# Optimization experiments

Hardware: AMD Instinct MI355X
Metric: run time of the kernel (lower is better)

Reference implementation:

```python
import jax, jax.numpy as jnp
import numpy as np
from jax import lax

B, N, H, D = 4, 384, 8, 5          # graphs, nodes/graph, heads, max multi-hop dist
NE, E_TOT, DH, L = 2048, 8192, 256, 10  # edges/graph, total real edges, d_hidden, curve samples
N_SPATIAL, N_EDGE_DIST = 64, 128


def _bn(x, g, b):
    # eval-mode BatchNorm1d (running_mean=0, running_var=1): affine only
    return x * g + b


def _conv1d(x, w):
    # x: [E, C, L], w: [O, I, 3], SAME padding, stride 1
    return lax.conv_general_dilated(x, w, (1,), 'SAME',
                                    dimension_numbers=('NCH', 'OIH', 'NCH'))


def setup_inputs() -> dict:
    key = jax.random.key(0)
    ks = iter(jax.random.split(key, 64))
    nrm = lambda shape, s=0.02: jax.random.normal(next(ks), shape, jnp.float32) * s
    std = 0.02 / np.sqrt(12.0)  # init_params with n_layer=12 for Linear weights
    inp = {}
    inp['attn_bias'] = jax.random.normal(next(ks), (B, N + 1, N + 1), jnp.float32)
    inp['spatial_pos'] = jax.random.randint(next(ks), (B, N, N), 0, N_SPATIAL)
    inp['d2_dist'] = jax.random.normal(next(ks), (B, N, N, 32), jnp.float32)
    inp['a3_dist'] = jax.random.normal(next(ks), (B, N, N, 32), jnp.float32)
    inp['edge_data'] = jax.random.normal(next(ks), (E_TOT, L, 7), jnp.float32)
    inp['edge_path'] = jax.random.randint(next(ks), (B, N, N, D), 0, NE + 1)
    inp['edge_padding_mask'] = jnp.zeros((B, NE), bool)  # all real edges
    inp['src'] = jax.random.randint(next(ks), (E_TOT,), 0, B * N)
    inp['dst'] = jax.random.randint(next(ks), (E_TOT,), 0, B * N)
    inp['node_data'] = jax.random.normal(next(ks), (B * N, DH), jnp.float32)
    # --- parameters ---
    inp['spatial_emb'] = nrm((N_SPATIAL, H)).at[0].set(0.0)  # padding_idx=0
    inp['t_virtual'] = nrm((1, H))
    inp['w_d2'] = nrm((H, 32), std); inp['b_d2'] = jnp.zeros((H,), jnp.float32)
    inp['w_a3'] = nrm((H, 32), std); inp['b_a3'] = jnp.zeros((H,), jnp.float32)
    inp['cw1'] = nrm((64, 7, 3), std);  inp['cg1'] = jnp.ones((64,));  inp['cb1'] = jnp.zeros((64,))
    inp['cw2'] = nrm((128, 64, 3), std); inp['cg2'] = jnp.ones((128,)); inp['cb2'] = jnp.zeros((128,))
    inp['cw3'] = nrm((256, 128, 3), std); inp['cg3'] = jnp.ones((256,)); inp['cb3'] = jnp.zeros((256,))
    inp['cw_out'] = nrm((H, 256), std)
    # _EdgeConv (UV-Net style): proj Linear(d_hidden->H), MLP(H->64->H), BN, GIN eps
    inp['wp'] = nrm((H, DH), std); inp['bp'] = jnp.zeros((H,))
    inp['w1'] = nrm((64, H), std); inp['b1'] = jnp.zeros((64,))
    inp['g1'] = jnp.ones((64,)); inp['bb1'] = jnp.zeros((64,))
    inp['w2'] = nrm((H, 64), std); inp['b2'] = jnp.zeros((H,))
    inp['g_out'] = jnp.ones((H,)); inp['bb_out'] = jnp.zeros((H,))
    inp['eps'] = jnp.zeros((), jnp.float32)
    inp['edge_dis_w'] = nrm((N_EDGE_DIST * H * H, 1))
    return inp


def reference(attn_bias, spatial_pos, d2_dist, a3_dist, edge_data, edge_path,
              edge_padding_mask, src, dst, node_data, spatial_emb, t_virtual,
              w_d2, b_d2, w_a3, b_a3, cw1, cg1, cb1, cw2, cg2, cb2, cw3, cg3, cb3,
              cw_out, wp, bp, w1, b1, g1, bb1, w2, b2, g_out, bb_out, eps, edge_dis_w):
    gab = jnp.repeat(attn_bias[:, None], H, axis=1)            # [B,H,N+1,N+1]
    spb = spatial_emb[spatial_pos]                              # [B,N,N,H]
    d2b = d2_dist @ w_d2.T + b_d2                               # [B,N,N,H]
    a3b = a3_dist @ w_a3.T + b_a3                               # [B,N,N,H]
    # CurveEncoder on per-edge curve samples
    x = jnp.transpose(edge_data, (0, 2, 1))                     # [E,7,L]
    x = jax.nn.leaky_relu(_bn(_conv1d(x, cw1), cg1[:, None], cb1[:, None]))
    x = jax.nn.leaky_relu(_bn(_conv1d(x, cw2), cg2[:, None], cb2[:, None]))
    x = jax.nn.leaky_relu(_bn(_conv1d(x, cw3), cg3[:, None], cb3[:, None]))
    ef = jnp.mean(x, axis=-1) @ cw_out.T                        # [E,H]
    # _EdgeConv: combine endpoint node features with edge features
    proj = node_data @ wp.T + bp                                # [B*N,H]
    h = (1.0 + eps) * ef + proj[src] + proj[dst]
    h = jax.nn.relu(_bn(h @ w1.T + b1, g1, bb1)) @ w2.T + b2
    edge_out = jax.nn.relu(_bn(h, g_out, bb_out))               # [E,H]
    # scatter real-edge features into padded table (row NE stays zero = padding)
    valid = (~edge_padding_mask).reshape(-1)                    # [B*NE]
    gidx = jnp.maximum(jnp.cumsum(valid) - 1, 0)
    vals = jnp.where(valid[:, None], edge_out[gidx], 0.0).reshape(B, NE, H)
    edge_feature = jnp.zeros((B, NE + 1, H), edge_out.dtype).at[:, :NE].set(vals)
    # gather along multi-hop paths, per-distance head mixing (bmm), normalize
    ep = edge_path.reshape(B, N * N * D)
    edge_input = jax.vmap(lambda f, p: f[p])(edge_feature, ep)  # [B,N*N*D,H]
    edge_input = edge_input.reshape(B, N, N, D, H)
    wdis = edge_dis_w.reshape(-1, H, H)[:D]                     # [D,H,H]
    edge_input = jnp.einsum('bijdh,dhk->bijdk', edge_input, wdis)
    sp = jnp.where(spatial_pos == 0, 1, spatial_pos)
    sp = jnp.where(sp > 1, sp - 1, sp)
    sp = jnp.clip(sp, 0, D)
    edge_bias = edge_input.sum(-2) / sp[..., None].astype(edge_input.dtype)
    inner = spb + d2b + a3b + edge_bias                         # [B,N,N,H]
    gab = gab.at[:, :, 1:, 1:].add(jnp.transpose(inner, (0, 3, 1, 2)))
    t = t_virtual.reshape(1, H, 1)
    gab = gab.at[:, :, 1:, 0].add(t)
    gab = gab.at[:, :, 0, :].add(t)
    return gab + attn_bias[:, None]
```

## Files before the change

### kernel.cpp

```cpp
#include <hip/hip_runtime.h>

#define NB    4
#define NNODE 384
#define NH    8
#define ND    5
#define NEDGE 2048
#define NEP1  2049
#define ETOT  8192
#define DHID  256
#define NP1   385
#define SQ1   (NP1*NP1)
#define NPOS  98304
#define NPOS2 (NPOS + 2)
#define NCELL (NB*NNODE*NNODE)

typedef __attribute__((ext_vector_type(8)))  short short8;
typedef __attribute__((ext_vector_type(16))) float float16;

__device__ __forceinline__ unsigned short f2bf(float f) {
    union { float f; unsigned int u; } v; v.f = f;
    unsigned int u = v.u;
    return (unsigned short)((u + 0x7FFFu + ((u >> 16) & 1u)) >> 16);
}
__device__ __forceinline__ float bf2f(unsigned short s) {
    union { unsigned int u; float f; } v; v.u = ((unsigned int)s) << 16; return v.f;
}
__device__ __forceinline__ unsigned pkbf(float a, float b) {
    return (unsigned)f2bf(a) | ((unsigned)f2bf(b) << 16);
}
__device__ __forceinline__ short8 mk8(unsigned a, unsigned b, unsigned c, unsigned d) {
    union { unsigned u[4]; short8 s; } x; x.u[0]=a; x.u[1]=b; x.u[2]=c; x.u[3]=d; return x.s;
}
__device__ __forceinline__ float leaky(float v) { return v > 0.f ? v : 0.01f * v; }
__device__ __forceinline__ float16 zero16() {
    float16 z;
#pragma unroll
    for (int i = 0; i < 16; ++i) z[i] = 0.f;
    return z;
}
__device__ __forceinline__ void gl_lds16(const void* g, void* l) {
    __builtin_amdgcn_global_load_lds(
        (const __attribute__((address_space(1))) unsigned int*)g,
        (__attribute__((address_space(3))) unsigned int*)l,
        16, 0, 0);
}

__global__ __launch_bounds__(256) void prep_kernel(
    const float* __restrict__ cw1, const float* __restrict__ cw2, const float* __restrict__ cw3,
    const float* __restrict__ cw_out,
    const float* __restrict__ node_data, const float* __restrict__ wp, const float* __restrict__ bp,
    unsigned short* __restrict__ W1f, unsigned short* __restrict__ W2f, unsigned short* __restrict__ W3f,
    unsigned short* __restrict__ Wof,
    float* __restrict__ proj, float* __restrict__ edge_feature)
{
    int gid = blockIdx.x * 256 + threadIdx.x;
    if (gid < 98304) {
        int j = gid & 7, lane = (gid >> 3) & 63, blk = gid >> 9;
        int ks = blk & 7, tp = (blk >> 3) % 3, mt = blk / 24;
        int oc = mt * 32 + (lane & 31);
        int ic = ks * 16 + (lane >> 5) * 8 + j;
        W3f[gid] = f2bf(cw3[(oc * 128 + ic) * 3 + tp]);
    } else if (gid < 122880) {
        int f = gid - 98304;
        int j = f & 7, lane = (f >> 3) & 63, blk = f >> 9;
        int ks = blk & 3, tp = (blk >> 2) % 3, mt = blk / 12;
        int oc = mt * 32 + (lane & 31);
        int ic = ks * 16 + (lane >> 5) * 8 + j;
        W2f[f] = f2bf(cw2[(oc * 64 + ic) * 3 + tp]);
    } else if (gid < 124928) {
        int f = gid - 122880;
        int j = f & 7, lane = (f >> 3) & 63, blk = f >> 9;
        int ks = blk & 1, mt = blk >> 1;
        int oc = mt * 32 + (lane & 31);
        int k = ks * 16 + (lane >> 5) * 8 + j;
        int tp = k >> 3, c = k & 7;
        float v = (tp < 3 && c < 7) ? cw1[oc * 21 + c * 3 + tp] : 0.f;
        W1f[f] = f2bf(v);
    } else if (gid < 137216) {
        int f = gid - 124928;
        int v = f >> 3, h = f & 7;
        const float4* nd4 = (const float4*)(node_data + (size_t)v * DHID);
        const float4* ww4 = (const float4*)(wp + (size_t)h * DHID);
        float s0 = 0.f, s1 = 0.f, s2 = 0.f, s3 = 0.f;
#pragma unroll 4
        for (int c = 0; c < 64; c += 4) {
            float4 x0 = nd4[c+0], y0 = ww4[c+0];
            float4 x1 = nd4[c+1], y1 = ww4[c+1];
            float4 x2 = nd4[c+2], y2 = ww4[c+2];
            float4 x3 = nd4[c+3], y3 = ww4[c+3];
            s0 += x0.x*y0.x + x0.y*y0.y + x0.z*y0.z + x0.w*y0.w;
            s1 += x1.x*y1.x + x1.y*y1.y + x1.z*y1.z + x1.w*y1.w;
            s2 += x2.x*y2.x + x2.y*y2.y + x2.z*y2.z + x2.w*y2.w;
            s3 += x3.x*y3.x + x3.y*y3.y + x3.z*y3.z + x3.w*y3.w;
        }
        proj[f] = bp[h] + (s0 + s1) + (s2 + s3);
    } else if (gid < 137248) {
        int f = gid - 137216;
        int b = f >> 3, h = f & 7;
        edge_feature[((size_t)b * NEP1 + NEDGE) * NH + h] = 0.f;
    } else if (gid < 145440) {
        int f = gid - 137248;
        int j = f & 7, lane = (f >> 3) & 63, g = f >> 9;
        int m = lane & 31;
        int k = g * 16 + (lane >> 5) * 8 + j;
        Wof[f] = (m < 8) ? f2bf(cw_out[m * 256 + k]) : (unsigned short)0;
    }
}

#define X0_GROWS 8
__global__ __launch_bounds__(256) void pack_kernel(
    const float* __restrict__ edge_data,
    unsigned short* __restrict__ X0buf, unsigned short* __restrict__ X1buf,
    unsigned short* __restrict__ X2buf)
{
    int gid = blockIdx.x * 256 + threadIdx.x;
    const int NX0 = (NPOS + 2 * X0_GROWS) * 8;
    if (gid < NX0) {
        int row = gid >> 3, ch = gid & 7;
        int pos = row - X0_GROWS;
        unsigned short v = 0;
        if (pos >= 0 && pos < NPOS && ch < 7) {
            int pm = pos % 12;
            if (pm >= 1 && pm <= 10)
                v = f2bf(edge_data[(size_t)(pos / 12) * 70 + (pm - 1) * 7 + ch]);
        }
        X0buf[gid] = v;
    } else if (gid < NX0 + 128) {
        int f = gid - NX0;
        int p = f >> 5, rest = f & 31;
        int row = (rest >> 4) ? (NPOS + 1) : 0, col = rest & 15;
        X1buf[((size_t)p * NPOS2 + row) * 16 + col] = 0;
    } else if (gid < NX0 + 128 + 256) {
        int f = gid - NX0 - 128;
        int p = f >> 5, rest = f & 31;
        int row = (rest >> 4) ? (NPOS + 1) : 0, col = rest & 15;
        X2buf[((size_t)p * NPOS2 + row) * 16 + col] = 0;
    }
}

__global__ __launch_bounds__(256, 4) void conv1_kernel(
    const unsigned short* __restrict__ X0, const unsigned short* __restrict__ W1f,
    const float* __restrict__ cg1, const float* __restrict__ cb1,
    unsigned short* __restrict__ X1)
{
    const int t = threadIdx.x, wv = t >> 6, lane = t & 63;
    const int q = lane >> 5, n = lane & 31;
    const int pos = blockIdx.x * 128 + wv * 32 + n;

    float16 acc0 = zero16(), acc1 = zero16();
#pragma unroll
    for (int ks = 0; ks < 2; ++ks) {
        short8 b  = *(const short8*)(X0 + (pos - 1 + 2 * ks + q) * 8);
        short8 a0 = *(const short8*)(W1f + ((0 * 2 + ks) * 64 + lane) * 8);
        short8 a1 = *(const short8*)(W1f + ((1 * 2 + ks) * 64 + lane) * 8);
        acc0 = __builtin_amdgcn_mfma_f32_32x32x16_bf16(a0, b, acc0, 0, 0, 0);
        acc1 = __builtin_amdgcn_mfma_f32_32x32x16_bf16(a1, b, acc1, 0, 0, 0);
    }
    int pm = pos % 12;
    bool valid = (pm != 0) && (pm != 11);
#pragma unroll
    for (int mt = 0; mt < 2; ++mt) {
        const float16& acc = mt ? acc1 : acc0;
#pragma unroll
        for (int r2 = 0; r2 < 4; ++r2) {
            int oc0 = mt * 32 + 8 * r2 + 4 * q;
            float4 g4 = *(const float4*)(cg1 + oc0);
            float4 b4 = *(const float4*)(cb1 + oc0);
            unsigned short uu[4];
            uu[0] = valid ? f2bf(leaky(acc[r2*4+0] * g4.x + b4.x)) : (unsigned short)0;
            uu[1] = valid ? f2bf(leaky(acc[r2*4+1] * g4.y + b4.y)) : (unsigned short)0;
            uu[2] = valid ? f2bf(leaky(acc[r2*4+2] * g4.z + b4.z)) : (unsigned short)0;
            uu[3] = valid ? f2bf(leaky(acc[r2*4+3] * g4.w + b4.w)) : (unsigned short)0;
            uint2 pk; pk.x = uu[0] | ((unsigned)uu[1] << 16); pk.y = uu[2] | ((unsigned)uu[3] << 16);
            *(uint2*)(void*)(X1 + ((size_t)(oc0 >> 4) * NPOS2 + pos + 1) * 16 + (oc0 & 15)) = pk;
        }
    }
}

__global__ __launch_bounds__(256, 4) void conv2_kernel(
    const unsigned short* __restrict__ X1, const unsigned short* __restrict__ W2f,
    const float* __restrict__ cg2, const float* __restrict__ cb2,
    unsigned short* __restrict__ X2)
{
    __shared__ __align__(16) unsigned short sB[4][1568];
    const int t = threadIdx.x, wv = t >> 6, lane = t & 63;
    const int q = lane >> 5, n = lane & 31;
    const int base = blockIdx.x * 96;
    const int cbase = (wv < 3) ? wv * 64 : 132;

#pragma unroll
    for (int ks = 0; ks < 4; ++ks)
        gl_lds16(X1 + ((size_t)ks * NPOS2 + base) * 16 + (cbase + lane) * 8,
                 &sB[ks][cbase * 8]);

    float16 acc[3];
#pragma unroll
    for (int nt = 0; nt < 3; ++nt) acc[nt] = zero16();

    __syncthreads();

#pragma unroll
    for (int ks = 0; ks < 4; ++ks)
#pragma unroll
        for (int tp = 0; tp < 3; ++tp) {
            short8 a = *(const short8*)(W2f + (((wv * 3 + tp) * 4 + ks) * 64 + lane) * 8);
#pragma unroll
            for (int nt = 0; nt < 3; ++nt) {
                short8 b = *(const short8*)(&sB[ks][(nt * 32 + n + tp) * 16 + q * 8]);
                acc[nt] = __builtin_amdgcn_mfma_f32_32x32x16_bf16(a, b, acc[nt], 0, 0, 0);
            }
        }

#pragma unroll
    for (int nt = 0; nt < 3; ++nt) {
        int pos = base + nt * 32 + n;
        int pm = pos % 12;
        bool valid = (pm != 0) && (pm != 11);
#pragma unroll
        for (int r2 = 0; r2 < 4; ++r2) {
            int oc0 = wv * 32 + 8 * r2 + 4 * q;
            float4 g4 = *(const float4*)(cg2 + oc0);
            float4 b4 = *(const float4*)(cb2 + oc0);
            unsigned short uu[4];
            uu[0] = valid ? f2bf(leaky(acc[nt][r2*4+0] * g4.x + b4.x)) : (unsigned short)0;
            uu[1] = valid ? f2bf(leaky(acc[nt][r2*4+1] * g4.y + b4.y)) : (unsigned short)0;
            uu[2] = valid ? f2bf(leaky(acc[nt][r2*4+2] * g4.z + b4.z)) : (unsigned short)0;
            uu[3] = valid ? f2bf(leaky(acc[nt][r2*4+3] * g4.w + b4.w)) : (unsigned short)0;
            uint2 pk; pk.x = uu[0] | ((unsigned)uu[1] << 16); pk.y = uu[2] | ((unsigned)uu[3] << 16);
            *(uint2*)(void*)(X2 + ((size_t)(oc0 >> 4) * NPOS2 + pos + 1) * 16 + (oc0 & 15)) = pk;
        }
    }
}

__global__ __launch_bounds__(256, 3) void conv3_kernel(
    const unsigned short* __restrict__ X2, const unsigned short* __restrict__ W3f,
    const unsigned short* __restrict__ Wof,
    const float* __restrict__ cg3, const float* __restrict__ cb3,
    const int* __restrict__ src, const int* __restrict__ dst,
    const float* __restrict__ w1, const float* __restrict__ b1,
    const float* __restrict__ g1, const float* __restrict__ bb1,
    const float* __restrict__ w2, const float* __restrict__ b2,
    const float* __restrict__ g_out, const float* __restrict__ bb_out,
    const float* __restrict__ eps, const float* __restrict__ proj,
    float* __restrict__ edge_feature)
{
    __shared__ __align__(16) unsigned char smem3[25088];
    unsigned short* sB = (unsigned short*)smem3;
    float* fs = (float*)smem3;
    const int t = threadIdx.x, wv = t >> 6, lane = t & 63;
    const int q = lane >> 5, n = lane & 31;
    const int base = blockIdx.x * 96;
    const int cbase = (wv < 3) ? wv * 64 : 132;

#pragma unroll
    for (int ks = 0; ks < 8; ++ks)
        gl_lds16(X2 + ((size_t)ks * NPOS2 + base) * 16 + (cbase + lane) * 8,
                 &sB[ks * 1568 + cbase * 8]);

    float16 acc[2][3];
#pragma unroll
    for (int i = 0; i < 2; ++i)
#pragma unroll
        for (int nt = 0; nt < 3; ++nt) acc[i][nt] = zero16();

    __syncthreads();

#pragma unroll
    for (int ks = 0; ks < 8; ++ks)
#pragma unroll
        for (int tp = 0; tp < 3; ++tp) {
            short8 a0 = *(const short8*)(W3f + ((((wv*2+0) * 3 + tp) * 8 + ks) * 64 + lane) * 8);
            short8 a1 = *(const short8*)(W3f + ((((wv*2+1) * 3 + tp) * 8 + ks) * 64 + lane) * 8);
#pragma unroll
            for (int nt = 0; nt < 3; ++nt) {
                short8 b = *(const short8*)(&sB[ks * 1568 + (nt * 32 + n + tp) * 16 + q * 8]);
                acc[0][nt] = __builtin_amdgcn_mfma_f32_32x32x16_bf16(a0, b, acc[0][nt], 0, 0, 0);
                acc[1][nt] = __builtin_amdgcn_mfma_f32_32x32x16_bf16(a1, b, acc[1][nt], 0, 0, 0);
            }
        }

    __syncthreads();

    short8 wof[4];
#pragma unroll
    for (int g = 0; g < 4; ++g)
        wof[g] = *(const short8*)(Wof + ((wv * 4 + g) * 64 + lane) * 8);

#pragma unroll
    for (int nt = 0; nt < 3; ++nt) {
        int pm = (nt * 32 + n) % 12;
        bool valid = (pm != 0) && (pm != 11);
        float16 p = zero16();
#pragma unroll
        for (int i = 0; i < 2; ++i) {
            int mt = wv * 2 + i;
            float av[16];
#pragma unroll
            for (int r2 = 0; r2 < 4; ++r2) {
                int oc0 = mt * 32 + 8 * r2 + 4 * q;
                float4 g4 = *(const float4*)(cg3 + oc0);
                float4 b4 = *(const float4*)(cb3 + oc0);
                av[r2*4+0] = valid ? leaky(acc[i][nt][r2*4+0] * g4.x + b4.x) : 0.f;
                av[r2*4+1] = valid ? leaky(acc[i][nt][r2*4+1] * g4.y + b4.y) : 0.f;
                av[r2*4+2] = valid ? leaky(acc[i][nt][r2*4+2] * g4.z + b4.z) : 0.f;
                av[r2*4+3] = valid ? leaky(acc[i][nt][r2*4+3] * g4.w + b4.w) : 0.f;
            }
            unsigned pk[8], op[8];
#pragma unroll
            for (int z = 0; z < 8; ++z) pk[z] = pkbf(av[2*z], av[2*z+1]);
#pragma unroll
            for (int z = 0; z < 8; ++z) op[z] = __shfl_xor((int)pk[z], 32);
            short8 f0 = q == 0 ? mk8(pk[0], pk[1], op[0], op[1])
                               : mk8(op[2], op[3], pk[2], pk[3]);
            short8 f1 = q == 0 ? mk8(pk[4], pk[5], op[4], op[5])
                               : mk8(op[6], op[7], pk[6], pk[7]);
            p = __builtin_amdgcn_mfma_f32_32x32x16_bf16(wof[i*2+0], f0, p, 0, 0, 0);
            p = __builtin_amdgcn_mfma_f32_32x32x16_bf16(wof[i*2+1], f1, p, 0, 0, 0);
        }
        float4 st = make_float4(p[0], p[1], p[2], p[3]);
        *(float4*)&fs[((wv * 96) + nt * 32 + n) * 8 + 4 * q] = st;
    }
    __syncthreads();

    if (t < 64) {
        int e = t >> 3, h = t & 7;
        float s = 0.f;
#pragma unroll
        for (int w = 0; w < 4; ++w)
#pragma unroll 4
            for (int l = 0; l < 12; ++l) s += fs[(w * 96 + e * 12 + l) * 8 + h];
        float efv = 0.1f * s;
        int ge = blockIdx.x * 8 + e;
        fs[3072 + e * 8 + h] = (1.f + eps[0]) * efv
                             + proj[src[ge] * NH + h] + proj[dst[ge] * NH + h];
    }
    __syncthreads();

#pragma unroll
    for (int bb = 0; bb < 512; bb += 256) {
        int idx = bb + t;
        int e = idx >> 6, o = idx & 63;
        float a = b1[o];
#pragma unroll
        for (int h = 0; h < 8; ++h) a += fs[3072 + e * 8 + h] * w1[o * 8 + h];
        float v = a * g1[o] + bb1[o];
        fs[3136 + e * 64 + o] = v > 0.f ? v : 0.f;
    }
    __syncthreads();

    if (t < 64) {
        int e = t >> 3, h = t & 7;
        float a = b2[h];
#pragma unroll 8
        for (int o = 0; o < 64; ++o) a += fs[3136 + e * 64 + o] * w2[h * 64 + o];
        float v = a * g_out[h] + bb_out[h];
        v = v > 0.f ? v : 0.f;
        int ge = blockIdx.x * 8 + e;
        int b = ge >> 11, el2 = ge & (NEDGE - 1);
        edge_feature[((size_t)b * NEP1 + el2) * NH + h] = v;
    }
}

__global__ __launch_bounds__(256) void eins_kernel(
    const float* __restrict__ d2_dist, const float* __restrict__ a3_dist,
    const float* __restrict__ w_d2, const float* __restrict__ w_a3,
    unsigned short* __restrict__ acc8)
{
    __shared__ __align__(16) float s_wd2[256];
    __shared__ __align__(16) float s_wa3[256];
    int t = threadIdx.x;
    s_wd2[t] = w_d2[t]; s_wa3[t] = w_a3[t];
    __syncthreads();

    const int part = t & 7;
    const bool pb0 = part & 1, pb1 = (part >> 1) & 1, pb2 = (part >> 2) & 1;
    size_t cell = (size_t)blockIdx.x * 32 + (t >> 3);

    float4 vd = ((const float4*)(d2_dist + cell * 32))[part];
    float4 va = ((const float4*)(a3_dist + cell * 32))[part];

    float acc[8];
#pragma unroll
    for (int h = 0; h < 8; ++h) {
        float4 w4 = ((const float4*)s_wd2)[h * 8 + part];
        float4 v4 = ((const float4*)s_wa3)[h * 8 + part];
        acc[h] = vd.x*w4.x + vd.y*w4.y + vd.z*w4.z + vd.w*w4.w
               + va.x*v4.x + va.y*v4.y + va.z*v4.z + va.w*v4.w;
    }
    float y0 = (pb0 ? acc[1] : acc[0]) + __shfl_xor(pb0 ? acc[0] : acc[1], 1, 64);
    float y1 = (pb0 ? acc[3] : acc[2]) + __shfl_xor(pb0 ? acc[2] : acc[3], 1, 64);
    float y2 = (pb0 ? acc[5] : acc[4]) + __shfl_xor(pb0 ? acc[4] : acc[5], 1, 64);
    float y3 = (pb0 ? acc[7] : acc[6]) + __shfl_xor(pb0 ? acc[6] : acc[7], 1, 64);
    float z0 = (pb1 ? y1 : y0) + __shfl_xor(pb1 ? y0 : y1, 2, 64);
    float z1 = (pb1 ? y3 : y2) + __shfl_xor(pb1 ? y2 : y3, 2, 64);
    float rr = (pb2 ? z1 : z0) + __shfl_xor(pb2 ? z0 : z1, 4, 64);

    acc8[cell * 8 + part] = f2bf(rr);
}

__global__ __launch_bounds__(256) void tbl_kernel(
    const float* __restrict__ edge_feature, const float* __restrict__ edge_dis_w,
    float* __restrict__ T)
{
    int idx = blockIdx.x * 256 + threadIdx.x;
    if (idx >= NEP1 * 8) return;
    int pi = idx >> 3, k = idx & 7;
    int d = blockIdx.y, b = blockIdx.z;
    const float* ef = edge_feature + ((size_t)b * NEP1 + pi) * NH;
    const float* w  = edge_dis_w + d * 64 + k;
    float s = 0.f;
#pragma unroll
    for (int h = 0; h < 8; ++h) s += ef[h] * w[h * 8];
    T[(((size_t)b * ND + d) * NEP1 + pi) * 8 + k] = s;
}

__global__ __launch_bounds__(256) void bias_kernel(
    const float* __restrict__ attn_bias, const int* __restrict__ spatial_pos,
    const int* __restrict__ edge_path,
    const float* __restrict__ spatial_emb, const float* __restrict__ t_virtual,
    const float* __restrict__ b_d2, const float* __restrict__ b_a3,
    const float* __restrict__ Tbl, const unsigned short* __restrict__ acc8,
    float* __restrict__ out)
{
    __shared__ float s_emb[512];
    __shared__ float s_t[8], s_bd2[8], s_ba3[8];

    int t = threadIdx.x;
    for (int i = t; i < 512; i += 256) s_emb[i] = spatial_emb[i];
    if (t < 8) { s_t[t] = t_virtual[t]; s_bd2[t] = b_d2[t]; s_ba3[t] = b_a3[t]; }
    __syncthreads();

    int gc = blockIdx.x * 32 + (t >> 3);
    int part = t & 7;
    if (gc >= NB * SQ1) return;
    int b   = gc / SQ1;
    int rem = gc % SQ1;
    int i = rem / NP1, j = rem % NP1;

    float base = 2.f * attn_bias[gc];
    bool border = (i == 0) || (j == 0);
    int r = border ? 0 : i - 1, c = border ? 0 : j - 1;
    size_t nidx = ((size_t)b * NNODE + r) * NNODE + c;
    int sp = spatial_pos[nidx];

    float accv = bf2f(acc8[nidx * 8 + part]);

    float edp = 0.f;
    const int* ep = edge_path + nidx * ND;
    const float* Tb = Tbl + (size_t)b * (ND * NEP1 * 8);
#pragma unroll
    for (int d = 0; d < ND; ++d) {
        int pi = ep[d];
        edp += Tb[((size_t)d * NEP1 + pi) * 8 + part];
    }
    int spd = (sp == 0) ? 1 : sp;
    spd = (spd > 1) ? spd - 1 : spd;
    spd = (spd > ND) ? ND : spd;
    float inv = 1.f / (float)spd;

    float val = border ? (base + s_t[part])
                       : (base + accv + edp * inv
                          + s_emb[sp * 8 + part] + s_bd2[part] + s_ba3[part]);
    out[((size_t)b * NH + part) * SQ1 + (size_t)i * NP1 + j] = val;
}

extern "C" void kernel_launch(void* const* d_in, const int* in_sizes, int n_in,
                              void* d_out, int out_size, void* d_ws, size_t ws_size,
                              hipStream_t stream)
{
    const float* attn_bias   = (const float*)d_in[0];
    const int*   spatial_pos = (const int*)  d_in[1];
    const float* d2_dist     = (const float*)d_in[2];
    const float* a3_dist     = (const float*)d_in[3];
    const float* edge_data   = (const float*)d_in[4];
    const int*   edge_path   = (const int*)  d_in[5];
    const int*   src         = (const int*)  d_in[7];
    const int*   dst         = (const int*)  d_in[8];
    const float* node_data   = (const float*)d_in[9];
    const float* spatial_emb = (const float*)d_in[10];
    const float* t_virtual   = (const float*)d_in[11];
    const float* w_d2        = (const float*)d_in[12];
    const float* b_d2        = (const float*)d_in[13];
    const float* w_a3        = (const float*)d_in[14];
    const float* b_a3        = (const float*)d_in[15];
    const float* cw1         = (const float*)d_in[16];
    const float* cg1         = (const float*)d_in[17];
    const float* cb1         = (const float*)d_in[18];
    const float* cw2         = (const float*)d_in[19];
    const float* cg2         = (const float*)d_in[20];
    const float* cb2         = (const float*)d_in[21];
    const float* cw3         = (const float*)d_in[22];
    const float* cg3         = (const float*)d_in[23];
    const float* cb3         = (const float*)d_in[24];
    const float* cw_out      = (const float*)d_in[25];
    const float* wp          = (const float*)d_in[26];
    const float* bp          = (const float*)d_in[27];
    const float* w1          = (const float*)d_in[28];
    const float* b1          = (const float*)d_in[29];
    const float* g1          = (const float*)d_in[30];
    const float* bb1         = (const float*)d_in[31];
    const float* w2          = (const float*)d_in[32];
    const float* b2          = (const float*)d_in[33];
    const float* g_out       = (const float*)d_in[34];
    const float* bb_out      = (const float*)d_in[35];
    const float* eps         = (const float*)d_in[36];
    const float* edge_dis_w  = (const float*)d_in[37];

    float*          proj  = (float*)d_ws;
    float*          ef    = proj + NB * NNODE * NH;
    unsigned short* W1f   = (unsigned short*)(ef + NB * NEP1 * NH);
    unsigned short* W2f   = W1f + 2048;
    unsigned short* W3f   = W2f + 24576;
    unsigned short* Wof   = W3f + 98304;
    unsigned short* X0buf = Wof + 8192;
    unsigned short* X1buf = X0buf + (size_t)(NPOS + 2 * X0_GROWS) * 8;
    unsigned short* X2buf = X1buf + (size_t)4 * NPOS2 * 16;
    unsigned short* X0 = X0buf + X0_GROWS * 8;
    float*          Tbl   = (float*)X0buf;
    unsigned short* acc8  = X1buf;

    prep_kernel<<<569, 256, 0, stream>>>(cw1, cw2, cw3, cw_out, node_data, wp, bp,
                                         W1f, W2f, W3f, Wof, proj, ef);
    pack_kernel<<<3074, 256, 0, stream>>>(edge_data, X0buf, X1buf, X2buf);

    conv1_kernel<<<NPOS / 128, 256, 0, stream>>>(X0, W1f, cg1, cb1, X1buf);
    conv2_kernel<<<NPOS / 96, 256, 0, stream>>>(X1buf, W2f, cg2, cb2, X2buf);

    eins_kernel<<<NCELL / 32, 256, 0, stream>>>(d2_dist, a3_dist, w_d2, w_a3, acc8);

    conv3_kernel<<<NPOS / 96, 256, 0, stream>>>(X2buf, W3f, Wof, cg3, cb3,
                                                src, dst, w1, b1, g1, bb1,
                                                w2, b2, g_out, bb_out, eps,
                                                proj, ef);

    dim3 tgrid((NEP1 * 8 + 255) / 256, ND, NB);
    tbl_kernel<<<tgrid, 256, 0, stream>>>(ef, edge_dis_w, Tbl);

    int nbias = (NB * SQ1 * 8 + 255) / 256;
    bias_kernel<<<nbias, 256, 0, stream>>>(
        attn_bias, spatial_pos, edge_path,
        spatial_emb, t_virtual, b_d2, b_a3,
        Tbl, acc8, (float*)d_out);
}
```

Measured before the change: 370.1 us.

## Make einsum kernel persistent with register weights and prefetch; one cell per bias thread

The d2/a3 einsum kernel now keeps its weights in registers instead of shared memory. It runs a grid-stride loop over 8 cells per thread and prefetches the next cell's inputs. The bias kernel now assigns one output cell per thread instead of one head per thread. That thread reads all 8 heads with vector loads of acc8 and the Tbl rows, which cuts repeated index loads (spatial_pos, edge_path, attn_bias) by a factor of 8. The cost is that the eight output stores per thread are strided by SQ1 across heads, and more registers are used per thread.

```diff
diff --git a/kernel.cpp b/kernel.cpp
--- a/kernel.cpp
+++ b/kernel.cpp
@@ -366,36 +366,42 @@
     const float* __restrict__ w_d2, const float* __restrict__ w_a3,
     unsigned short* __restrict__ acc8)
 {
-    __shared__ __align__(16) float s_wd2[256];
-    __shared__ __align__(16) float s_wa3[256];
-    int t = threadIdx.x;
-    s_wd2[t] = w_d2[t]; s_wa3[t] = w_a3[t];
-    __syncthreads();
-
-    const int part = t & 7;
+    const int t = threadIdx.x, part = t & 7;
+    float4 wd[8], wa[8];
+#pragma unroll
+    for (int h = 0; h < 8; ++h) {
+        wd[h] = *(const float4*)(w_d2 + h * 32 + part * 4);
+        wa[h] = *(const float4*)(w_a3 + h * 32 + part * 4);
+    }
     const bool pb0 = part & 1, pb1 = (part >> 1) & 1, pb2 = (part >> 2) & 1;
+    const size_t stride = 73728;
     size_t cell = (size_t)blockIdx.x * 32 + (t >> 3);
 
     float4 vd = ((const float4*)(d2_dist + cell * 32))[part];
     float4 va = ((const float4*)(a3_dist + cell * 32))[part];
-
-    float acc[8];
-#pragma unroll
-    for (int h = 0; h < 8; ++h) {
-        float4 w4 = ((const float4*)s_wd2)[h * 8 + part];
-        float4 v4 = ((const float4*)s_wa3)[h * 8 + part];
-        acc[h] = vd.x*w4.x + vd.y*w4.y + vd.z*w4.z + vd.w*w4.w
-               + va.x*v4.x + va.y*v4.y + va.z*v4.z + va.w*v4.w;
-    }
-    float y0 = (pb0 ? acc[1] : acc[0]) + __shfl_xor(pb0 ? acc[0] : acc[1], 1, 64);
-    float y1 = (pb0 ? acc[3] : acc[2]) + __shfl_xor(pb0 ? acc[2] : acc[3], 1, 64);
-    float y2 = (pb0 ? acc[5] : acc[4]) + __shfl_xor(pb0 ? acc[4] : acc[5], 1, 64);
-    float y3 = (pb0 ? acc[7] : acc[6]) + __shfl_xor(pb0 ? acc[6] : acc[7], 1, 64);
-    float z0 = (pb1 ? y1 : y0) + __shfl_xor(pb1 ? y0 : y1, 2, 64);
-    float z1 = (pb1 ? y3 : y2) + __shfl_xor(pb1 ? y2 : y3, 2, 64);
-    float rr = (pb2 ? z1 : z0) + __shfl_xor(pb2 ? z0 : z1, 4, 64);
-
-    acc8[cell * 8 + part] = f2bf(rr);
+#pragma unroll 1
+    for (int it = 0; it < 8; ++it) {
+        float4 nvd = vd, nva = va;
+        if (it < 7) {
+            nvd = ((const float4*)(d2_dist + (cell + stride) * 32))[part];
+            nva = ((const float4*)(a3_dist + (cell + stride) * 32))[part];
+        }
+        float acc[8];
+#pragma unroll
+        for (int h = 0; h < 8; ++h)
+            acc[h] = vd.x*wd[h].x + vd.y*wd[h].y + vd.z*wd[h].z + vd.w*wd[h].w
+                   + va.x*wa[h].x + va.y*wa[h].y + va.z*wa[h].z + va.w*wa[h].w;
+        float y0 = (pb0 ? acc[1] : acc[0]) + __shfl_xor(pb0 ? acc[0] : acc[1], 1, 64);
+        float y1 = (pb0 ? acc[3] : acc[2]) + __shfl_xor(pb0 ? acc[2] : acc[3], 1, 64);
+        float y2 = (pb0 ? acc[5] : acc[4]) + __shfl_xor(pb0 ? acc[4] : acc[5], 1, 64);
+        float y3 = (pb0 ? acc[7] : acc[6]) + __shfl_xor(pb0 ? acc[6] : acc[7], 1, 64);
+        float z0 = (pb1 ? y1 : y0) + __shfl_xor(pb1 ? y0 : y1, 2, 64);
+        float z1 = (pb1 ? y3 : y2) + __shfl_xor(pb1 ? y2 : y3, 2, 64);
+        float rr = (pb2 ? z1 : z0) + __shfl_xor(pb2 ? z0 : z1, 4, 64);
+        acc8[cell * 8 + part] = f2bf(rr);
+        cell += stride;
+        vd = nvd; va = nva;
+    }
 }
 
 __global__ __launch_bounds__(256) void tbl_kernel(
@@ -422,46 +428,50 @@
     const float* __restrict__ Tbl, const unsigned short* __restrict__ acc8,
     float* __restrict__ out)
 {
-    __shared__ float s_emb[512];
-    __shared__ float s_t[8], s_bd2[8], s_ba3[8];
-
+    __shared__ __align__(16) float s_emb[512];
     int t = threadIdx.x;
     for (int i = t; i < 512; i += 256) s_emb[i] = spatial_emb[i];
-    if (t < 8) { s_t[t] = t_virtual[t]; s_bd2[t] = b_d2[t]; s_ba3[t] = b_a3[t]; }
-    __syncthreads();
-
-    int gc = blockIdx.x * 32 + (t >> 3);
-    int part = t & 7;
+    __syncthreads();
+
+    int gc = blockIdx.x * 256 + t;
     if (gc >= NB * SQ1) return;
-    int b   = gc / SQ1;
-    int rem = gc % SQ1;
+    int b = gc / SQ1, rem = gc % SQ1;
     int i = rem / NP1, j = rem % NP1;
-
     float base = 2.f * attn_bias[gc];
     bool border = (i == 0) || (j == 0);
-    int r = border ? 0 : i - 1, c = border ? 0 : j - 1;
-    size_t nidx = ((size_t)b * NNODE + r) * NNODE + c;
-    int sp = spatial_pos[nidx];
-
-    float accv = bf2f(acc8[nidx * 8 + part]);
-
-    float edp = 0.f;
-    const int* ep = edge_path + nidx * ND;
-    const float* Tb = Tbl + (size_t)b * (ND * NEP1 * 8);
-#pragma unroll
-    for (int d = 0; d < ND; ++d) {
-        int pi = ep[d];
-        edp += Tb[((size_t)d * NEP1 + pi) * 8 + part];
-    }
-    int spd = (sp == 0) ? 1 : sp;
-    spd = (spd > 1) ? spd - 1 : spd;
-    spd = (spd > ND) ? ND : spd;
-    float inv = 1.f / (float)spd;
-
-    float val = border ? (base + s_t[part])
-                       : (base + accv + edp * inv
-                          + s_emb[sp * 8 + part] + s_bd2[part] + s_ba3[part]);
-    out[((size_t)b * NH + part) * SQ1 + (size_t)i * NP1 + j] = val;
+
+    float res[8];
+    if (border) {
+#pragma unroll
+        for (int h = 0; h < 8; ++h) res[h] = base + t_virtual[h];
+    } else {
+        size_t nidx = ((size_t)b * NNODE + (i - 1)) * NNODE + (j - 1);
+        int sp = spatial_pos[nidx];
+        union { uint4 u; unsigned short s[8]; } aa;
+        aa.u = *(const uint4*)(acc8 + nidx * 8);
+        const int* ep = edge_path + nidx * ND;
+        const float* Tb = Tbl + (size_t)b * (ND * NEP1 * 8);
+        float edp[8] = {0,0,0,0,0,0,0,0};
+#pragma unroll
+        for (int d = 0; d < ND; ++d) {
+            const float* r = Tb + ((size_t)d * NEP1 + ep[d]) * 8;
+            float4 r0 = *(const float4*)r;
+            float4 r1 = *(const float4*)(r + 4);
+            edp[0] += r0.x; edp[1] += r0.y; edp[2] += r0.z; edp[3] += r0.w;
+            edp[4] += r1.x; edp[5] += r1.y; edp[6] += r1.z; edp[7] += r1.w;
+        }
+        int spd = (sp == 0) ? 1 : sp;
+        spd = (spd > 1) ? spd - 1 : spd;
+        spd = (spd > ND) ? ND : spd;
+        float inv = 1.f / (float)spd;
+        const float* em = s_emb + sp * 8;
+#pragma unroll
+        for (int h = 0; h < 8; ++h)
+            res[h] = base + bf2f(aa.s[h]) + edp[h] * inv + em[h] + b_d2[h] + b_a3[h];
+    }
+#pragma unroll
+    for (int h = 0; h < 8; ++h)
+        out[((size_t)b * NH + h) * SQ1 + rem] = res[h];
 }
 
 extern "C" void kernel_launch(void* const* d_in, const int* in_sizes, int n_in,
@@ -526,7 +536,7 @@
     conv1_kernel<<<NPOS / 128, 256, 0, stream>>>(X0, W1f, cg1, cb1, X1buf);
     conv2_kernel<<<NPOS / 96, 256, 0, stream>>>(X1buf, W2f, cg2, cb2, X2buf);
 
-    eins_kernel<<<NCELL / 32, 256, 0, stream>>>(d2_dist, a3_dist, w_d2, w_a3, acc8);
+    eins_kernel<<<2304, 256, 0, stream>>>(d2_dist, a3_dist, w_d2, w_a3, acc8);
 
     conv3_kernel<<<NPOS / 96, 256, 0, stream>>>(X2buf, W3f, Wof, cg3, cb3,
                                                 src, dst, w1, b1, g1, bb1,
@@ -536,7 +546,7 @@
     dim3 tgrid((NEP1 * 8 + 255) / 256, ND, NB);
     tbl_kernel<<<tgrid, 256, 0, stream>>>(ef, edge_dis_w, Tbl);
 
-    int nbias = (NB * SQ1 * 8 + 255) / 256;
+    int nbias = (NB * SQ1 + 255) / 256;
     bias_kernel<<<nbias, 256, 0, stream>>>(
         attn_bias, spatial_pos, edge_path,
         spatial_emb, t_virtual, b_d2, b_a3,
```

Result: faster. 358.7 us (-3.1%).
